# Performance work log

Hardware: AMD Instinct MI355X
Metric: run time of the kernel (lower is better)

Reference implementation:

```python
import jax, jax.numpy as jnp
import numpy as np

# Config mirroring RegionExtractor(__init__ defaults, stage='rcnn')
MIN_SIZE = 25.0
IOU_THRESH = 0.3
SCORE_THRESH = 0.001  # applied as box_score_thresh inside the wrapped FRCNN
MAX_DET = 100         # max_detections_per_image
IMG_SIZE = 800.0
B, N = 8, 2048


def setup_inputs() -> dict:
    key = jax.random.key(0)
    k_c, k_wh, k_s = jax.random.split(key, 3)
    # synthesize realistic xyxy boxes inside an 800x800 image
    centers = jax.random.uniform(k_c, (B, N, 2), minval=0.0, maxval=IMG_SIZE)
    wh = jax.random.uniform(k_wh, (B, N, 2), minval=1.0, maxval=250.0)
    x1y1 = jnp.clip(centers - wh / 2, 0.0, IMG_SIZE)
    x2y2 = jnp.clip(centers + wh / 2, 0.0, IMG_SIZE)
    boxes = jnp.concatenate([x1y1, x2y2], axis=-1).astype(jnp.float32)  # [B,N,4]
    scores = jax.random.uniform(k_s, (B, N), dtype=jnp.float32)          # [B,N]
    return {"boxes": boxes, "scores": scores}


def _box_iou(a, b):
    # a: [N,4], b: [N,4] xyxy -> [N,N] IoU (torchvision convention, no +1)
    area_a = (a[:, 2] - a[:, 0]) * (a[:, 3] - a[:, 1])
    area_b = (b[:, 2] - b[:, 0]) * (b[:, 3] - b[:, 1])
    lt = jnp.maximum(a[:, None, :2], b[None, :, :2])
    rb = jnp.minimum(a[:, None, 2:], b[None, :, 2:])
    wh = jnp.clip(rb - lt, 0.0)
    inter = wh[..., 0] * wh[..., 1]
    return inter / (area_a[:, None] + area_b[None, :] - inter)


def _process_image(boxes, scores):
    # boxes [N,4], scores [N] -> (out [K,4], mask [K])
    n = boxes.shape[0]
    w = boxes[:, 2] - boxes[:, 0]
    h = boxes[:, 3] - boxes[:, 1]
    # remove_small_boxes + score threshold (box_score_thresh in wrapped FRCNN)
    valid = (w >= MIN_SIZE) & (h >= MIN_SIZE) & (scores >= SCORE_THRESH)
    order = jnp.argsort(-jnp.where(valid, scores, -jnp.inf))  # desc, invalid last
    b = boxes[order]
    v = valid[order]
    sup = _box_iou(b, b) > IOU_THRESH  # [N,N]
    idx = jnp.arange(n)

    def body(i, keep):
        suppressed = jnp.any(keep & sup[:, i] & (idx < i))
        return keep.at[i].set(v[i] & ~suppressed)

    keep = jax.lax.fori_loop(0, n, body, jnp.zeros(n, dtype=bool))
    # keep is in score order already; take first MAX_DET kept boxes
    rank = jnp.cumsum(keep) - 1
    sel = keep & (rank < MAX_DET)
    tgt = jnp.where(sel, rank, MAX_DET)  # dump non-selected into scratch row
    out = jnp.zeros((MAX_DET + 1, 4), boxes.dtype).at[tgt].set(b)[:MAX_DET]
    num_kept = jnp.minimum(jnp.sum(keep), MAX_DET)
    mask = jnp.arange(MAX_DET) < num_kept
    return out, mask


def reference(boxes, scores):
    # Per-image filter + NMS + top-k, batched via vmap (padded fixed-shape output:
    # original returns a ragged [sum_k,5]; here rows with mask==False are padding).
    out, mask = jax.vmap(_process_image)(boxes, scores)  # [B,K,4], [B,K]
    b = boxes.shape[0]
    img_idx = jnp.repeat(jnp.arange(b, dtype=boxes.dtype), MAX_DET)[:, None]  # [B*K,1]
    regions = jnp.concatenate([img_idx, out.reshape(b * MAX_DET, 4)], axis=1)  # [B*K,5]
    return regions, mask.reshape(-1)
```

## Files before the change

kernel.cpp:

```cpp
#include <hip/hip_runtime.h>

#define NBOX   2048
#define HALF   1024
#define MAXDET 100
#define NIMG   8
#define POOL   256
#define IOU_MID 0x1.333335p-2

typedef unsigned long long u64;

__device__ __forceinline__ u64 shx64(u64 v, int m) {
    int lo = __shfl_xor((int)(unsigned int)v, m, 64);
    int hi = __shfl_xor((int)(unsigned int)(v >> 32), m, 64);
    return ((u64)(unsigned int)hi << 32) | (unsigned int)lo;
}
__device__ __forceinline__ u64 cmpsel(u64 mine, u64 part, bool take_max) {
    return ((mine > part) == take_max) ? mine : part;
}
__device__ __forceinline__ u64 readlane64(u64 v, int l) {
    unsigned int lo = (unsigned int)__builtin_amdgcn_readlane((int)(unsigned int)v, l);
    unsigned int hi = (unsigned int)__builtin_amdgcn_readlane((int)(v >> 32), l);
    return ((u64)hi << 32) | lo;
}
__device__ __forceinline__ u64 mkkey(float4 v, float s, int i) {
    bool valid = ((v.z - v.x) >= 25.0f) && ((v.w - v.y) >= 25.0f) && (s >= 0.001f);
    unsigned int sk = valid ? __float_as_uint(s) : 0u;
    return ((u64)sk << 32) | (unsigned int)(~i);
}

__global__ __launch_bounds__(512) void k_all(
    const float* __restrict__ boxes, const float* __restrict__ scores,
    float* __restrict__ out)
{
    __shared__ u64    bufA[NBOX];
    __shared__ u64    bufB[NBOX];
    __shared__ u64    supRow[POOL * 4];
    __shared__ float4 sbox[POOL];
    __shared__ u64    mA[POOL], mB[POOL];
    __shared__ u64    validW[4];
    __shared__ u64    pminS;
    __shared__ int    kposL[MAXDET];
    __shared__ float4 leadersB[MAXDET];
    __shared__ float  leadersA[MAXDET];

    const int g    = threadIdx.x;
    const int lane = g & 63;
    const int wv   = g >> 6;
    const int img  = blockIdx.x;
    const float4* bb4 = (const float4*)boxes + img * NBOX;
    const float*  ss  = scores + img * NBOX;

    const int e0 = 2 * g;
    u64 k0, k1, k2, k3;
    { float4 v = bb4[e0];            k0 = mkkey(v, ss[e0],            e0);            }
    { float4 v = bb4[e0 + 1];        k1 = mkkey(v, ss[e0 + 1],        e0 + 1);        }
    { float4 v = bb4[HALF + e0];     k2 = mkkey(v, ss[HALF + e0],     HALF + e0);     }
    { float4 v = bb4[HALF + e0 + 1]; k3 = mkkey(v, ss[HALF + e0 + 1], HALF + e0 + 1); }

#define SWAP1(a, b, D) { if ((D) ? ((a) < (b)) : ((a) > (b))) { u64 t_ = (a); (a) = (b); (b) = t_; } }
    { bool D = ((g & 1) == 0); SWAP1(k0, k1, D) SWAP1(k2, k3, D) }
    for (int KB = 2; KB <= 64; KB <<= 1) {
        bool D = ((g & KB) == 0);
        for (int m = KB >> 1; m >= 1; m >>= 1) {
            bool tm = (D == ((lane & m) == 0));
            k0 = cmpsel(k0, shx64(k0, m), tm);
            k1 = cmpsel(k1, shx64(k1, m), tm);
            k2 = cmpsel(k2, shx64(k2, m), tm);
            k3 = cmpsel(k3, shx64(k3, m), tm);
        }
        SWAP1(k0, k1, D) SWAP1(k2, k3, D)
    }
    int sp = 0;
    for (int K = 256; K <= 1024; K <<= 1) {
        bool D = ((e0 & K) == 0);
        for (int j = K >> 1; j >= 128; j >>= 1) {
            u64* buf = (sp & 1) ? bufB : bufA;
            ++sp;
            buf[e0] = k0;        buf[e0 + 1] = k1;
            buf[HALF + e0] = k2; buf[HALF + e0 + 1] = k3;
            __syncthreads();
            int pe = e0 ^ j;
            u64 p0 = buf[pe], p1 = buf[pe + 1];
            u64 p2 = buf[HALF + pe], p3 = buf[HALF + pe + 1];
            bool tm = (D == ((e0 & j) == 0));
            k0 = cmpsel(k0, p0, tm); k1 = cmpsel(k1, p1, tm);
            k2 = cmpsel(k2, p2, tm); k3 = cmpsel(k3, p3, tm);
        }
        for (int m = 32; m >= 1; m >>= 1) {
            bool tm = (D == ((lane & m) == 0));
            k0 = cmpsel(k0, shx64(k0, m), tm);
            k1 = cmpsel(k1, shx64(k1, m), tm);
            k2 = cmpsel(k2, shx64(k2, m), tm);
            k3 = cmpsel(k3, shx64(k3, m), tm);
        }
        SWAP1(k0, k1, D) SWAP1(k2, k3, D)
    }
    bufA[e0] = k0;        bufA[e0 + 1] = k1;
    bufA[HALF + e0] = k2; bufA[HALF + e0 + 1] = k3;
    __syncthreads();

    const u64* hk = bufA;

    u64 c = 0;
    if (g < POOL) {
        u64 a  = hk[g];
        u64 bq = hk[HALF + (POOL - 1 - g)];
        c = (a > bq) ? a : bq;
        mA[g] = c;
    }
    __syncthreads();
    if (g < POOL) { c = cmpsel(c, mA[g ^ 128], (g & 128) == 0); mB[g] = c; }
    __syncthreads();
    if (g < POOL) {
        c = cmpsel(c, mB[g ^ 64], (g & 64) == 0);
        for (int m = 32; m >= 1; m >>= 1)
            c = cmpsel(c, shx64(c, m), (lane & m) == 0);
        unsigned int idx = ~(unsigned int)c;
        float4 v = bb4[idx];
        sbox[g] = v;
        u64 bal = __ballot(((unsigned int)(c >> 32)) != 0u);
        if (lane == 0) validW[wv] = bal;
        if (g == POOL - 1) pminS = c;
    }
    __syncthreads();

    float4 cb[4];
    float  ca[4];
#pragma unroll
    for (int w = 0; w < 4; ++w) {
        float4 v = sbox[(w << 6) + lane];
        cb[w] = v;
        ca[w] = (v.z - v.x) * (v.w - v.y);
    }

    for (int r = 0; r < POOL / 8; ++r) {
        int i = (r << 3) + wv;
        float4 Li = sbox[i];
        float La = (Li.z - Li.x) * (Li.w - Li.y);
        int w0 = i >> 6;
#pragma unroll
        for (int w = 0; w < 4; ++w) {
            if (w >= w0) {
                int j0 = (w << 6) + lane;
                float iw = fminf(Li.z, cb[w].z) - fmaxf(Li.x, cb[w].x);
                float ih = fminf(Li.w, cb[w].w) - fmaxf(Li.y, cb[w].y);
                iw = fmaxf(iw, 0.0f);
                ih = fmaxf(ih, 0.0f);
                float inter = iw * ih;
                float denom = (La + ca[w]) - inter;
                bool hit = (j0 > i) && ((double)inter > IOU_MID * (double)denom);
                u64 bits = __ballot(hit);
                if (lane == 0) supRow[(i << 2) + w] = bits;
            }
        }
    }
    __syncthreads();

    if (g >= 64) return;

    float* regions = out;
    float* maskv   = out + (size_t)NIMG * MAXDET * 5;

    u64 rd0 = supRow[(((0 << 6) + lane) << 2) + 0];
    u64 rd1 = supRow[(((1 << 6) + lane) << 2) + 1];
    u64 rd2 = supRow[(((2 << 6) + lane) << 2) + 2];
    u64 rd3 = supRow[(((3 << 6) + lane) << 2) + 3];

    int nkept = 0;
    u64 pend = 0;
#pragma unroll
    for (int s = 0; s < 4; ++s) {
        u64 rds = (s == 0) ? rd0 : (s == 1) ? rd1 : (s == 2) ? rd2 : rd3;
        u64 mcur = validW[s] & ~readlane64(pend, s);
        int n0 = nkept;
        while (mcur != 0ULL) {
            int il = (int)__builtin_ctzll(mcur);
            if (lane == 0) kposL[nkept] = (s << 6) + il;
            nkept++;
            if (nkept >= MAXDET) break;
            u64 rowS = readlane64(rds, il);
            mcur = (mcur & (mcur - 1)) & ~rowS;
        }
        if (nkept >= MAXDET) break;
        if (s < 3) {
            for (int t = n0 + (lane >> 2); t < nkept; t += 16)
                pend |= supRow[(kposL[t] << 2) + (lane & 3)];
            pend |= shx64(pend, 4);
            pend |= shx64(pend, 8);
            pend |= shx64(pend, 16);
            pend |= shx64(pend, 32);
        }
    }

    for (int t = lane; t < nkept; t += 64) {
        int ip = kposL[t];
        float4 v = sbox[ip];
        float* rr = regions + ((size_t)(img * MAXDET + t)) * 5;
        rr[0] = (float)img; rr[1] = v.x; rr[2] = v.y; rr[3] = v.z; rr[4] = v.w;
        maskv[img * MAXDET + t] = 1.0f;
        leadersB[t] = v;
        leadersA[t] = (v.z - v.x) * (v.w - v.y);
    }

    if (nkept < MAXDET) {
        u64 pmin = pminS;
        int q0 = 0, q1 = 0;
        while (q0 < HALF && hk[q0] >= pmin) ++q0;
        while (q1 < HALF && hk[HALF + q1] >= pmin) ++q1;
        while (nkept < MAXDET) {
            u64 h0 = (q0 < HALF) ? hk[q0] : 0;
            u64 h1 = (q1 < HALF) ? hk[HALF + q1] : 0;
            u64 hmax = (h0 > h1) ? h0 : h1;
            if ((unsigned int)(hmax >> 32) == 0u) break;
            if (hmax == h0) ++q0; else ++q1;
            unsigned int idx = ~(unsigned int)hmax;
            float4 v = bb4[idx];
            float varea = (v.z - v.x) * (v.w - v.y);
            bool sup = false;
            for (int t = lane; t < nkept; t += 64) {
                float4 Lb = leadersB[t];
                float  La = leadersA[t];
                float iw = fminf(Lb.z, v.z) - fmaxf(Lb.x, v.x);
                float ih = fminf(Lb.w, v.w) - fmaxf(Lb.y, v.y);
                iw = fmaxf(iw, 0.0f);
                ih = fmaxf(ih, 0.0f);
                float inter = iw * ih;
                float denom = (La + varea) - inter;
                if ((double)inter > IOU_MID * (double)denom) sup = true;
            }
            if (__ballot(sup) == 0ULL) {
                if (lane == 0) {
                    float* rr = regions + ((size_t)(img * MAXDET + nkept)) * 5;
                    rr[0] = (float)img; rr[1] = v.x; rr[2] = v.y; rr[3] = v.z; rr[4] = v.w;
                    maskv[img * MAXDET + nkept] = 1.0f;
                    leadersB[nkept] = v;
                    leadersA[nkept] = varea;
                }
                nkept++;
            }
        }
    }

    for (int r = nkept + lane; r < MAXDET; r += 64) {
        float* rr = regions + ((size_t)(img * MAXDET + r)) * 5;
        rr[0] = (float)img; rr[1] = 0.0f; rr[2] = 0.0f; rr[3] = 0.0f; rr[4] = 0.0f;
        maskv[img * MAXDET + r] = 0.0f;
    }
}

extern "C" void kernel_launch(void* const* d_in, const int* in_sizes, int n_in,
                              void* d_out, int out_size, void* d_ws, size_t ws_size,
                              hipStream_t stream) {
    const float* boxes  = (const float*)d_in[0];
    const float* scores = (const float*)d_in[1];
    float* out = (float*)d_out;
    k_all<<<NIMG, 512, 0, stream>>>(boxes, scores, out);
}
```

Baseline: 83.25 us.

## Batch NMS fallback: process 64 candidates per wavefront step with bitonic merge

The serial fallback that pulls one candidate at a time from two sorted halves is replaced by a wave-wide scheme. Each step bitonic-merges the next 64 keys from both halves. Every lane tests its own candidate against all current leaders, then the survivors are resolved in score order among themselves with ballots and readlane broadcasts. The pmin skip scans are also vectorised with ballot/popcount. This removes one-candidate-per-iteration latency when many fallback candidates are needed, at the cost of each lane looping over all leaders serially and doing wasted work when few candidates are needed.

```diff
diff --git a/kernel.cpp b/kernel.cpp
--- a/kernel.cpp
+++ b/kernel.cpp
@@ -21,6 +21,9 @@
     unsigned int lo = (unsigned int)__builtin_amdgcn_readlane((int)(unsigned int)v, l);
     unsigned int hi = (unsigned int)__builtin_amdgcn_readlane((int)(v >> 32), l);
     return ((u64)hi << 32) | lo;
+}
+__device__ __forceinline__ float readlanef(float v, int l) {
+    return __int_as_float(__builtin_amdgcn_readlane(__float_as_int(v), l));
 }
 __device__ __forceinline__ u64 mkkey(float4 v, float s, int i) {
     bool valid = ((v.z - v.x) >= 25.0f) && ((v.w - v.y) >= 25.0f) && (s >= 0.001f);
@@ -205,19 +208,36 @@
     if (nkept < MAXDET) {
         u64 pmin = pminS;
         int q0 = 0, q1 = 0;
-        while (q0 < HALF && hk[q0] >= pmin) ++q0;
-        while (q1 < HALF && hk[HALF + q1] >= pmin) ++q1;
-        while (nkept < MAXDET) {
-            u64 h0 = (q0 < HALF) ? hk[q0] : 0;
-            u64 h1 = (q1 < HALF) ? hk[HALF + q1] : 0;
-            u64 hmax = (h0 > h1) ? h0 : h1;
-            if ((unsigned int)(hmax >> 32) == 0u) break;
-            if (hmax == h0) ++q0; else ++q1;
-            unsigned int idx = ~(unsigned int)hmax;
+        for (;;) {
+            u64 key = (q0 + lane < HALF) ? hk[q0 + lane] : 0ULL;
+            int cnt = __popcll(__ballot(key >= pmin));
+            q0 += cnt;
+            if (cnt < 64) break;
+        }
+        for (;;) {
+            u64 key = (q1 + lane < HALF) ? hk[HALF + q1 + lane] : 0ULL;
+            int cnt = __popcll(__ballot(key >= pmin));
+            q1 += cnt;
+            if (cnt < 64) break;
+        }
+        while (nkept < MAXDET && (q0 < HALF || q1 < HALF)) {
+            u64 a  = (q0 + lane < HALF) ? hk[q0 + lane] : 0ULL;
+            int rb = q1 + (63 - lane);
+            u64 br = (rb < HALF) ? hk[HALF + rb] : 0ULL;
+            bool tookA = a > br;
+            u64 ck = tookA ? a : br;
+            int nA = __popcll(__ballot(tookA));
+            q0 += nA;
+            q1 += 64 - nA;
+            for (int m = 32; m >= 1; m >>= 1)
+                ck = cmpsel(ck, shx64(ck, m), (lane & m) == 0);
+            bool valid = ((unsigned int)(ck >> 32)) != 0u;
+            if (__ballot(valid) == 0ULL) break;
+            unsigned int idx = valid ? ~(unsigned int)ck : 0u;
             float4 v = bb4[idx];
-            float varea = (v.z - v.x) * (v.w - v.y);
+            float va = (v.z - v.x) * (v.w - v.y);
             bool sup = false;
-            for (int t = lane; t < nkept; t += 64) {
+            for (int t = 0; t < nkept; ++t) {
                 float4 Lb = leadersB[t];
                 float  La = leadersA[t];
                 float iw = fminf(Lb.z, v.z) - fmaxf(Lb.x, v.x);
@@ -225,18 +245,36 @@
                 iw = fmaxf(iw, 0.0f);
                 ih = fmaxf(ih, 0.0f);
                 float inter = iw * ih;
-                float denom = (La + varea) - inter;
+                float denom = (La + va) - inter;
                 if ((double)inter > IOU_MID * (double)denom) sup = true;
             }
-            if (__ballot(sup) == 0ULL) {
-                if (lane == 0) {
+            u64 surv = __ballot(valid && !sup);
+            while (surv != 0ULL && nkept < MAXDET) {
+                int ld = (int)__builtin_ctzll(surv);
+                float Lx = readlanef(v.x, ld), Ly = readlanef(v.y, ld);
+                float Lz = readlanef(v.z, ld), Lw = readlanef(v.w, ld);
+                float La = readlanef(va, ld);
+                if (lane == ld) {
                     float* rr = regions + ((size_t)(img * MAXDET + nkept)) * 5;
                     rr[0] = (float)img; rr[1] = v.x; rr[2] = v.y; rr[3] = v.z; rr[4] = v.w;
                     maskv[img * MAXDET + nkept] = 1.0f;
                     leadersB[nkept] = v;
-                    leadersA[nkept] = varea;
+                    leadersA[nkept] = va;
                 }
                 nkept++;
+                surv &= ~(1ULL << ld);
+                if (surv == 0ULL) break;
+                bool kill = false;
+                if ((surv >> lane) & 1ULL) {
+                    float iw = fminf(Lz, v.z) - fmaxf(Lx, v.x);
+                    float ih = fminf(Lw, v.w) - fmaxf(Ly, v.y);
+                    iw = fmaxf(iw, 0.0f);
+                    ih = fmaxf(ih, 0.0f);
+                    float inter = iw * ih;
+                    float denom = (La + va) - inter;
+                    kill = ((double)inter > IOU_MID * (double)denom);
+                }
+                surv &= ~__ballot(kill);
             }
         }
     }
```

Measured after the change: 83.92 us. About the same (+0.8%).
